# Kernel tuning notes

Measured on AMD Instinct MI355X. Metric: run time of the kernel, lower is better.

## Reference

```python
import jax, jax.numpy as jnp
import numpy as np

TOP_K = 2  # init_kwargs top_k


def setup_inputs() -> dict:
    key = jax.random.key(0)
    ks = jax.random.split(key, 6)
    B, S, D, H, E = 2, 2048, 768, 3072, 8
    sc = 0.02  # small init scale for weights
    rn = lambda k, shape, s: jax.random.normal(k, shape, dtype=jnp.float32) * s
    return {
        "x": rn(ks[0], (B, S, D), 1.0),
        "noise": rn(ks[1], (B, S, E), 1.0),  # stands in for torch.randn_like
        "Wg": rn(ks[2], (D, E), sc),
        "bg": jnp.zeros((E,), jnp.float32),
        "Wn": rn(ks[3], (D, E), sc),
        "bn": jnp.zeros((E,), jnp.float32),
        "W1": rn(ks[4], (E, D, H), sc),
        "b1": jnp.zeros((E, H), jnp.float32),
        "W2": rn(ks[5], (E, H, D), sc),
        "b2": jnp.zeros((E, D), jnp.float32),
    }


def reference(x, noise, Wg, bg, Wn, bn, W1, b1, W2, b2):
    E = Wg.shape[-1]
    # Noisy top-k gating: h = Wg(x) + randn * softplus(Wnoise(x))
    gate = x @ Wg + bg                      # [B,S,E]
    h = gate + noise * jax.nn.softplus(x @ Wn + bn)
    vals, idxs = jax.lax.top_k(h, TOP_K)    # [B,S,K]
    # softmax over -inf-filled logits == softmax over just the top-k values,
    # scattered back to expert slots (zeros elsewhere)
    probs = jax.nn.softmax(vals, axis=-1)   # [B,S,K]
    g = jnp.einsum("bsk,bske->bse", probs, jax.nn.one_hot(idxs, E, dtype=x.dtype))
    # Experts: dense batched FFN over all experts, then combine with gates.
    # (Mathematically identical to masked gather/scatter: g is 0 off top-k.)
    hid = jax.nn.relu(jnp.einsum("bsd,edh->ebsh", x, W1) + b1[:, None, None, :])
    y = jnp.einsum("ebsh,ehd->ebsd", hid, W2) + b2[:, None, None, :]
    out = jnp.einsum("ebsd,bse->bsd", y, g)  # gate-weighted combine
    return out
```

## Files before the change

kernel.cpp:

```cpp
#include <hip/hip_runtime.h>
#include <hip/hip_bf16.h>
#include <math.h>

#define TB 2
#define TS 2048
#define TT 4096
#define TD 768
#define TH 3072
#define TE 8
#define TASS (2*TT)

typedef short bf16x8 __attribute__((ext_vector_type(8)));
typedef float f32x4 __attribute__((ext_vector_type(4)));

__device__ inline unsigned short f2bfu(float f){
  __hip_bfloat16 h = __float2bfloat16(f);
  union { __hip_bfloat16 h; unsigned short u; } cv; cv.h = h; return cv.u;
}

#define GLOAD_LDS16(g, l) __builtin_amdgcn_global_load_lds( \
    (const __attribute__((address_space(1))) void*)(g), \
    (__attribute__((address_space(3))) void*)(l), 16, 0, 0)

__global__ __launch_bounds__(256) void cvt_x_kernel(const float* __restrict__ x,
                                                    unsigned short* __restrict__ xb){
  int i = blockIdx.x*256 + threadIdx.x;
  float4 v = reinterpret_cast<const float4*>(x)[i];
  ushort4 o;
  o.x = f2bfu(v.x); o.y = f2bfu(v.y); o.z = f2bfu(v.z); o.w = f2bfu(v.w);
  reinterpret_cast<ushort4*>(xb)[i] = o;
}

__global__ __launch_bounds__(256) void transpose_cvt_kernel(const float* __restrict__ in,
    unsigned short* __restrict__ out, int R, int C){
  __shared__ float tile[32][33];
  const size_t eoff = (size_t)blockIdx.z * R * C;
  int c0 = blockIdx.x*32, r0 = blockIdx.y*32;
  #pragma unroll
  for (int i=0;i<4;i++)
    tile[threadIdx.y + i*8][threadIdx.x] =
      in[eoff + (size_t)(r0 + threadIdx.y + i*8)*C + c0 + threadIdx.x];
  __syncthreads();
  #pragma unroll
  for (int i=0;i<4;i++)
    out[eoff + (size_t)(c0 + threadIdx.y + i*8)*R + r0 + threadIdx.x] =
      f2bfu(tile[threadIdx.x][threadIdx.y + i*8]);
}

__global__ __launch_bounds__(256) void gating_kernel(const float* __restrict__ x,
    const float* __restrict__ noise, const float* __restrict__ Wg, const float* __restrict__ bg,
    const float* __restrict__ Wn, const float* __restrict__ bn,
    int* __restrict__ top2i, float* __restrict__ top2p){
  const int wave = threadIdx.x >> 6;
  const int lane = threadIdx.x & 63;
  const int t = blockIdx.x*4 + wave;
  float sg[TE], sn[TE];
  #pragma unroll
  for (int e=0;e<TE;e++){ sg[e]=0.f; sn[e]=0.f; }
  const float* xr = x + (size_t)t*TD;
  for (int d = lane; d < TD; d += 64){
    float xv = xr[d];
    float4 g0 = reinterpret_cast<const float4*>(Wg + d*TE)[0];
    float4 g1 = reinterpret_cast<const float4*>(Wg + d*TE)[1];
    float4 n0 = reinterpret_cast<const float4*>(Wn + d*TE)[0];
    float4 n1 = reinterpret_cast<const float4*>(Wn + d*TE)[1];
    sg[0] += xv*g0.x; sg[1] += xv*g0.y; sg[2] += xv*g0.z; sg[3] += xv*g0.w;
    sg[4] += xv*g1.x; sg[5] += xv*g1.y; sg[6] += xv*g1.z; sg[7] += xv*g1.w;
    sn[0] += xv*n0.x; sn[1] += xv*n0.y; sn[2] += xv*n0.z; sn[3] += xv*n0.w;
    sn[4] += xv*n1.x; sn[5] += xv*n1.y; sn[6] += xv*n1.z; sn[7] += xv*n1.w;
  }
  #pragma unroll
  for (int m = 32; m >= 1; m >>= 1){
    #pragma unroll
    for (int e=0;e<TE;e++){
      sg[e] += __shfl_xor(sg[e], m, 64);
      sn[e] += __shfl_xor(sn[e], m, 64);
    }
  }
  if (lane == 0){
    float h[TE];
    #pragma unroll
    for (int e=0;e<TE;e++){
      float z = sn[e] + bn[e];
      float sp = fmaxf(z, 0.f) + log1pf(expf(-fabsf(z)));
      h[e] = sg[e] + bg[e] + noise[(size_t)t*TE + e] * sp;
    }
    int i0 = 0;
    #pragma unroll
    for (int e=1;e<TE;e++) if (h[e] > h[i0]) i0 = e;
    int i1 = (i0 == 0) ? 1 : 0;
    #pragma unroll
    for (int e=0;e<TE;e++) if (e != i0 && h[e] > h[i1]) i1 = e;
    float v0 = h[i0], v1 = h[i1];
    float p1 = 1.f / (1.f + expf(v0 - v1));
    float p0 = 1.f - p1;
    top2i[t*2]   = i0; top2i[t*2+1] = i1;
    top2p[t*2]   = p0; top2p[t*2+1] = p1;
  }
}

__global__ __launch_bounds__(512) void route_kernel(const int* __restrict__ top2i,
    int* __restrict__ counts, int* __restrict__ offs,
    int* __restrict__ rowlist, int* __restrict__ tokpos){
  const int w    = threadIdx.x >> 6;
  const int lane = threadIdx.x & 63;
  __shared__ int cnt_lds[TE];
  __shared__ int off_lds[TE+1];

  int cnt = 0;
  for (int base = 0; base < TASS; base += 64){
    int e = top2i[base + lane];
    unsigned long long m = __ballot(e == w);
    cnt += (int)__popcll(m);
  }
  if (lane == 0) cnt_lds[w] = cnt;
  __syncthreads();
  if (threadIdx.x == 0){
    int acc = 0;
    #pragma unroll
    for (int e=0;e<TE;e++){ off_lds[e] = acc; acc += cnt_lds[e]; }
    off_lds[TE] = acc;
    #pragma unroll
    for (int e=0;e<TE;e++){ counts[e] = cnt_lds[e]; offs[e] = off_lds[e]; }
    offs[TE] = acc;
  }
  __syncthreads();

  const unsigned long long below = (lane == 0) ? 0ull : (~0ull >> (64 - lane));
  int run = off_lds[w];
  for (int base = 0; base < TASS; base += 64){
    int e = top2i[base + lane];
    unsigned long long m = __ballot(e == w);
    if (e == w){
      int pos = run + (int)__popcll(m & below);
      rowlist[pos] = (base + lane) >> 1;
      tokpos[base + lane] = pos;
    }
    run += (int)__popcll(m);
  }
}

template<int KDIM, int NDIM, int NKS, bool GATHER, bool RELU_BF16>
__global__ __launch_bounds__(256) void gemm_moe(
    const unsigned short* __restrict__ A,
    const unsigned short* __restrict__ Bt,
    const float* __restrict__ bias,
    const int* __restrict__ rowlist,
    const int* __restrict__ offs,
    const int* __restrict__ counts,
    unsigned short* __restrict__ outbf,
    float* __restrict__ outf)
{
  const int zz   = blockIdx.z;
  const int e    = (NKS == 1) ? zz : (zz >> 1);
  const int kseg = (NKS == 1) ? 0  : (zz & 1);
  int cnt = counts[e];
  cnt = cnt < 0 ? 0 : (cnt > TASS ? TASS : cnt);
  const int mt  = blockIdx.y;
  if (mt*128 >= cnt) return;
  int off = offs[e];
  off = off < 0 ? 0 : (off > TASS ? TASS : off);
  const int nt  = blockIdx.x;
  constexpr int KLEN = KDIM / NKS;
  const int kbeg = kseg * KLEN;

  __shared__ alignas(64) unsigned short As[128*64];
  __shared__ alignas(64) unsigned short Bs[128*64];

  const int tid  = threadIdx.x;
  const int lane = tid & 63;
  const int w    = tid >> 6;
  const int wm   = w >> 1, wn = w & 1;

  f32x4 acc[4][4];
  {
    f32x4 z = {0.f, 0.f, 0.f, 0.f};
    #pragma unroll
    for (int i=0;i<4;i++)
      #pragma unroll
      for (int j=0;j<4;j++) acc[i][j] = z;
  }

  const unsigned short* Be = Bt + (size_t)e*NDIM*KDIM + (size_t)nt*128*KDIM;

  size_t a_src[4], b_src[4];
  #pragma unroll
  for (int i=0;i<4;i++){
    int c   = i*256 + tid;
    int row = c >> 3;
    int lc8 = (c & 7) ^ (row & 7);
    int grl = mt*128 + row;
    size_t grow;
    if (GATHER){
      int ridx = off + (grl < cnt ? grl : 0);
      ridx = ridx < TASS ? ridx : (TASS - 1);
      int rv = rowlist[ridx];
      rv = (rv >= 0 && rv < TT) ? rv : 0;
      grow = (size_t)rv;
    } else {
      size_t g = (size_t)off + (size_t)grl;
      grow = g < (size_t)TASS ? g : (size_t)(TASS - 1);
    }
    a_src[i] = grow * KDIM + (size_t)(lc8 << 3);
    b_src[i] = (size_t)row * KDIM + (size_t)(lc8 << 3);
  }

  const char* Asb = (const char*)As;
  const char* Bsb = (const char*)Bs;
  const int rxor  = (lane & 7) << 4;
  const int arow0 = wm*64 + (lane & 15);
  const int brow0 = wn*64 + (lane & 15);
  const int kgrp  = (lane >> 4) << 4;

  for (int k0 = kbeg; k0 < kbeg + KLEN; k0 += 64){
    #pragma unroll
    for (int i=0;i<4;i++){
      unsigned short* ab = &As[(i*256 + w*64) * 8];
      unsigned short* bb = &Bs[(i*256 + w*64) * 8];
      GLOAD_LDS16(A  + a_src[i] + k0, ab);
      GLOAD_LDS16(Be + b_src[i] + k0, bb);
    }
    __syncthreads();
    #pragma unroll
    for (int ks=0; ks<2; ++ks){
      const int kby = ks*64 + kgrp;
      bf16x8 af[4], bfr[4];
      #pragma unroll
      for (int f=0; f<4; ++f)
        af[f]  = *reinterpret_cast<const bf16x8*>(Asb + (arow0 + f*16)*128 + (kby ^ rxor));
      #pragma unroll
      for (int f=0; f<4; ++f)
        bfr[f] = *reinterpret_cast<const bf16x8*>(Bsb + (brow0 + f*16)*128 + (kby ^ rxor));
      #pragma unroll
      for (int fm=0; fm<4; ++fm)
        #pragma unroll
        for (int fn=0; fn<4; ++fn)
          acc[fm][fn] = __builtin_amdgcn_mfma_f32_16x16x32_bf16(af[fm], bfr[fn], acc[fm][fn], 0, 0, 0);
    }
    __syncthreads();
  }

  const float* be = bias + (size_t)e*NDIM + (size_t)nt*128;
  float* outseg = outf + (size_t)kseg * TASS * NDIM;
  #pragma unroll
  for (int fm=0; fm<4; ++fm){
    const int rbase = wm*64 + fm*16 + ((lane >> 4) << 2);
    #pragma unroll
    for (int fn=0; fn<4; ++fn){
      const int lc = wn*64 + fn*16 + (lane & 15);
      #pragma unroll
      for (int r=0; r<4; ++r){
        int lr = mt*128 + rbase + r;
        if (lr < cnt && off + lr < TASS){
          float v = acc[fm][fn][r];
          if (kseg == 0) v += be[lc];
          if (RELU_BF16){
            v = fmaxf(v, 0.f);
            outbf[(size_t)(off + lr)*NDIM + nt*128 + lc] = f2bfu(v);
          } else {
            outseg[(size_t)(off + lr)*NDIM + nt*128 + lc] = v;
          }
        }
      }
    }
  }
}

__global__ __launch_bounds__(256) void combine_kernel(const float* __restrict__ y0,
    const int* __restrict__ tokpos, const float* __restrict__ top2p,
    float* __restrict__ out, int ks2){
  int i = blockIdx.x*256 + threadIdx.x;
  int t  = i / (TD/4);
  int dc = i % (TD/4);
  int pa = tokpos[t*2], pb = tokpos[t*2+1];
  pa = (pa >= 0 && pa < TASS) ? pa : 0;
  pb = (pb >= 0 && pb < TASS) ? pb : 0;
  float wa = top2p[t*2], wb = top2p[t*2+1];
  float4 ya = reinterpret_cast<const float4*>(y0)[(size_t)pa*(TD/4) + dc];
  float4 yb = reinterpret_cast<const float4*>(y0)[(size_t)pb*(TD/4) + dc];
  if (ks2){
    const float* y1 = y0 + (size_t)TASS*TD;
    float4 za = reinterpret_cast<const float4*>(y1)[(size_t)pa*(TD/4) + dc];
    float4 zb = reinterpret_cast<const float4*>(y1)[(size_t)pb*(TD/4) + dc];
    ya.x += za.x; ya.y += za.y; ya.z += za.z; ya.w += za.w;
    yb.x += zb.x; yb.y += zb.y; yb.z += zb.z; yb.w += zb.w;
  }
  float4 o;
  o.x = wa*ya.x + wb*yb.x;
  o.y = wa*ya.y + wb*yb.y;
  o.z = wa*ya.z + wb*yb.z;
  o.w = wa*ya.w + wb*yb.w;
  reinterpret_cast<float4*>(out)[i] = o;
}

extern "C" void kernel_launch(void* const* d_in, const int* in_sizes, int n_in,
                              void* d_out, int out_size, void* d_ws, size_t ws_size,
                              hipStream_t stream){
  const float* x     = (const float*)d_in[0];
  const float* noise = (const float*)d_in[1];
  const float* Wg    = (const float*)d_in[2];
  const float* bg    = (const float*)d_in[3];
  const float* Wn    = (const float*)d_in[4];
  const float* bn    = (const float*)d_in[5];
  const float* W1    = (const float*)d_in[6];
  const float* b1    = (const float*)d_in[7];
  const float* W2    = (const float*)d_in[8];
  const float* b2    = (const float*)d_in[9];
  float* out = (float*)d_out;

  constexpr size_t SZ_XB   = (size_t)TT*TD*2;
  constexpr size_t SZ_W1T  = (size_t)TE*TH*TD*2;
  constexpr size_t SZ_W2T  = (size_t)TE*TD*TH*2;
  constexpr size_t SZ_HID  = (size_t)TASS*TH*2;
  constexpr size_t SZ_YE   = (size_t)TASS*TD*4;
  constexpr size_t SZ_SMALL= 2*256 + 4*((size_t)TT*2*4);
  constexpr size_t BASE_NEED = SZ_XB+SZ_W1T+SZ_W2T+SZ_HID+SZ_YE+SZ_SMALL + 4096;
  const int ks2 = (BASE_NEED + SZ_YE <= ws_size) ? 1 : 0;

  char* p = (char*)d_ws;
  auto alloc = [&](size_t bytes)->void*{
    void* r = (void*)p;
    p += (bytes + 255) & ~(size_t)255;
    return r;
  };
  unsigned short* xb  = (unsigned short*)alloc(SZ_XB);
  unsigned short* W1t = (unsigned short*)alloc(SZ_W1T);
  unsigned short* W2t = (unsigned short*)alloc(SZ_W2T);
  unsigned short* hid = (unsigned short*)alloc(SZ_HID);
  float* ye           = (float*)alloc(ks2 ? 2*SZ_YE : SZ_YE);
  int* counts  = (int*)alloc(TE*4);
  int* offs    = (int*)alloc((TE+1)*4);
  int* top2i   = (int*)alloc((size_t)TT*2*4);
  float* top2p = (float*)alloc((size_t)TT*2*4);
  int* rowlist = (int*)alloc((size_t)TASS*4);
  int* tokpos  = (int*)alloc((size_t)TT*2*4);
  if ((size_t)(p - (char*)d_ws) > ws_size) return;

  cvt_x_kernel<<<TT*TD/4/256, 256, 0, stream>>>(x, xb);
  transpose_cvt_kernel<<<dim3(TH/32, TD/32, TE), dim3(32,8), 0, stream>>>(W1, W1t, TD, TH);
  transpose_cvt_kernel<<<dim3(TD/32, TH/32, TE), dim3(32,8), 0, stream>>>(W2, W2t, TH, TD);
  gating_kernel<<<TT/4, 256, 0, stream>>>(x, noise, Wg, bg, Wn, bn, top2i, top2p);
  route_kernel<<<1, 512, 0, stream>>>(top2i, counts, offs, rowlist, tokpos);

  gemm_moe<TD, TH, 1, true,  true ><<<dim3(TH/128, 32, TE), 256, 0, stream>>>(
      xb, W1t, b1, rowlist, offs, counts, hid, nullptr);
  if (ks2){
    gemm_moe<TH, TD, 2, false, false><<<dim3(TD/128, 32, TE*2), 256, 0, stream>>>(
        hid, W2t, b2, nullptr, offs, counts, nullptr, ye);
  } else {
    gemm_moe<TH, TD, 1, false, false><<<dim3(TD/128, 32, TE), 256, 0, stream>>>(
        hid, W2t, b2, nullptr, offs, counts, nullptr, ye);
  }

  combine_kernel<<<TT*TD/4/256, 256, 0, stream>>>(ye, tokpos, top2p, out, ks2);
}
```

Before: 454.3 us.

## Double-buffer LDS tiles in MoE GEMM and cache routing indices in LDS

The MoE GEMM kernel now keeps two LDS buffers for A and B tiles and issues the async global-to-LDS loads for the next K step before running MFMAs on the current one. This overlaps memory latency with compute and drops one barrier per iteration. The route kernel also copies the top-2 expert indices into shared memory once instead of reading them from global memory twice per wave. The cost is double the LDS use per block, which may lower occupancy.

```diff
diff --git a/kernel.cpp b/kernel.cpp
--- a/kernel.cpp
+++ b/kernel.cpp
@@ -102,15 +102,19 @@
 __global__ __launch_bounds__(512) void route_kernel(const int* __restrict__ top2i,
     int* __restrict__ counts, int* __restrict__ offs,
     int* __restrict__ rowlist, int* __restrict__ tokpos){
+  __shared__ int e_lds[TASS];
+  __shared__ int cnt_lds[TE];
+  __shared__ int off_lds[TE+1];
+  for (int i = threadIdx.x; i < TASS/4; i += 512)
+    reinterpret_cast<int4*>(e_lds)[i] = reinterpret_cast<const int4*>(top2i)[i];
+  __syncthreads();
+
   const int w    = threadIdx.x >> 6;
   const int lane = threadIdx.x & 63;
-  __shared__ int cnt_lds[TE];
-  __shared__ int off_lds[TE+1];
 
   int cnt = 0;
   for (int base = 0; base < TASS; base += 64){
-    int e = top2i[base + lane];
-    unsigned long long m = __ballot(e == w);
+    unsigned long long m = __ballot(e_lds[base + lane] == w);
     cnt += (int)__popcll(m);
   }
   if (lane == 0) cnt_lds[w] = cnt;
@@ -129,7 +133,7 @@
   const unsigned long long below = (lane == 0) ? 0ull : (~0ull >> (64 - lane));
   int run = off_lds[w];
   for (int base = 0; base < TASS; base += 64){
-    int e = top2i[base + lane];
+    int e = e_lds[base + lane];
     unsigned long long m = __ballot(e == w);
     if (e == w){
       int pos = run + (int)__popcll(m & below);
@@ -161,11 +165,12 @@
   int off = offs[e];
   off = off < 0 ? 0 : (off > TASS ? TASS : off);
   const int nt  = blockIdx.x;
-  constexpr int KLEN = KDIM / NKS;
+  constexpr int KLEN   = KDIM / NKS;
+  constexpr int NSTEPS = KLEN / 64;
   const int kbeg = kseg * KLEN;
 
-  __shared__ alignas(64) unsigned short As[128*64];
-  __shared__ alignas(64) unsigned short Bs[128*64];
+  __shared__ alignas(64) unsigned short As[2][128*64];
+  __shared__ alignas(64) unsigned short Bs[2][128*64];
 
   const int tid  = threadIdx.x;
   const int lane = tid & 63;
@@ -205,22 +210,21 @@
     b_src[i] = (size_t)row * KDIM + (size_t)(lc8 << 3);
   }
 
-  const char* Asb = (const char*)As;
-  const char* Bsb = (const char*)Bs;
   const int rxor  = (lane & 7) << 4;
   const int arow0 = wm*64 + (lane & 15);
   const int brow0 = wn*64 + (lane & 15);
   const int kgrp  = (lane >> 4) << 4;
 
-  for (int k0 = kbeg; k0 < kbeg + KLEN; k0 += 64){
+  auto STAGE = [&](int buf, int k0){
     #pragma unroll
     for (int i=0;i<4;i++){
-      unsigned short* ab = &As[(i*256 + w*64) * 8];
-      unsigned short* bb = &Bs[(i*256 + w*64) * 8];
-      GLOAD_LDS16(A  + a_src[i] + k0, ab);
-      GLOAD_LDS16(Be + b_src[i] + k0, bb);
-    }
-    __syncthreads();
+      GLOAD_LDS16(A  + a_src[i] + k0, &As[buf][(i*256 + w*64) * 8]);
+      GLOAD_LDS16(Be + b_src[i] + k0, &Bs[buf][(i*256 + w*64) * 8]);
+    }
+  };
+  auto COMPUTE = [&](int buf){
+    const char* Asb = (const char*)&As[buf][0];
+    const char* Bsb = (const char*)&Bs[buf][0];
     #pragma unroll
     for (int ks=0; ks<2; ++ks){
       const int kby = ks*64 + kgrp;
@@ -237,8 +241,19 @@
         for (int fn=0; fn<4; ++fn)
           acc[fm][fn] = __builtin_amdgcn_mfma_f32_16x16x32_bf16(af[fm], bfr[fn], acc[fm][fn], 0, 0, 0);
     }
+  };
+
+  STAGE(0, kbeg);
+  __syncthreads();
+  int cur = 0;
+  #pragma unroll 2
+  for (int t = 0; t < NSTEPS-1; ++t){
+    STAGE(cur^1, kbeg + (t+1)*64);
+    COMPUTE(cur);
     __syncthreads();
-  }
+    cur ^= 1;
+  }
+  COMPUTE(cur);
 
   const float* be = bias + (size_t)e*NDIM + (size_t)nt*128;
   float* outseg = outf + (size_t)kseg * TASS * NDIM;
```

New measurement: 432.5 us. -4.8%, faster.
